# Kernel tuning notes

Measured on AMD Instinct MI355X. Metric: run time of the kernel, lower is better.

Reference implementation:

```python
import jax, jax.numpy as jnp
import numpy as np

N, E, F_IN, F_E, EMB, G = 25000, 100000, 32, 8, 32, 512


def _nnconv(x, src, dst, ea, w1, b1, w2, b2, root, bias):
    # edge MLP: [E,F_E] -> [E,16] -> [E, in*EMB] -> per-edge weight matrix [E,in,EMB]
    h = jax.nn.relu(ea @ w1 + b1)
    W = (h @ w2 + b2).reshape(ea.shape[0], x.shape[1], EMB)
    # gather source nodes, per-edge matmul, scatter-add to targets (PyG NNConv, aggr='add')
    msg = jnp.einsum('ei,eio->eo', x[src], W)
    agg = jax.ops.segment_sum(msg, dst, num_segments=x.shape[0])
    return agg + x @ root + bias


def _branch(x, ei, ea, p0, p1):
    x = jax.nn.relu(_nnconv(x, ei[0], ei[1], ea, *p0))
    x = jax.nn.relu(_nnconv(x, ei[0], ei[1], ea, *p1))
    return x


def setup_inputs() -> dict:
    key = jax.random.key(0)
    ks = iter(jax.random.split(key, 64))
    def rnd(shape, s=1.0):
        return jax.random.normal(next(ks), shape, dtype=jnp.float32) * s
    inp = {
        'x_p': rnd((N, F_IN)), 'x_d': rnd((N, F_IN)),
        'edge_attr_p': rnd((E, F_E)), 'edge_attr_d': rnd((E, F_E)),
        'edge_index_p': jax.random.randint(next(ks), (2, E), 0, N),
        'edge_index_d': jax.random.randint(next(ks), (2, E), 0, N),
        'batch_p': jnp.sort(jax.random.randint(next(ks), (N,), 0, G)),
        'batch_d': jnp.sort(jax.random.randint(next(ks), (N,), 0, G)),
    }
    for b in ('p', 'd'):
        inp[b + '_nn0_w1'] = rnd((F_E, 16), 0.1)
        inp[b + '_nn0_b1'] = rnd((16,), 0.1)
        inp[b + '_nn0_w2'] = rnd((16, F_IN * EMB), 0.1)
        inp[b + '_nn0_b2'] = rnd((F_IN * EMB,), 0.1)
        inp[b + '_root0'] = rnd((F_IN, EMB), 0.1)
        inp[b + '_bias0'] = rnd((EMB,), 0.1)
        inp[b + '_nn1_w1'] = rnd((F_E, 16), 0.1)
        inp[b + '_nn1_b1'] = rnd((16,), 0.1)
        inp[b + '_nn1_w2'] = rnd((16, EMB * EMB), 0.1)
        inp[b + '_nn1_b2'] = rnd((EMB * EMB,), 0.1)
        inp[b + '_root1'] = rnd((EMB, EMB), 0.1)
        inp[b + '_bias1'] = rnd((EMB,), 0.1)
    inp['lin0_w'] = rnd((2 * EMB, 2 * EMB), 0.1)
    inp['lin0_b'] = rnd((2 * EMB,), 0.1)
    inp['lin1_w'] = rnd((2 * EMB, 1), 0.1)
    inp['lin1_b'] = rnd((1,), 0.1)
    return inp


def reference(x_p, x_d, edge_attr_p, edge_attr_d, edge_index_p, edge_index_d, batch_p, batch_d,
              p_nn0_w1, p_nn0_b1, p_nn0_w2, p_nn0_b2, p_root0, p_bias0,
              p_nn1_w1, p_nn1_b1, p_nn1_w2, p_nn1_b2, p_root1, p_bias1,
              d_nn0_w1, d_nn0_b1, d_nn0_w2, d_nn0_b2, d_root0, d_bias0,
              d_nn1_w1, d_nn1_b1, d_nn1_w2, d_nn1_b2, d_root1, d_bias1,
              lin0_w, lin0_b, lin1_w, lin1_b):
    p0 = (p_nn0_w1, p_nn0_b1, p_nn0_w2, p_nn0_b2, p_root0, p_bias0)
    p1 = (p_nn1_w1, p_nn1_b1, p_nn1_w2, p_nn1_b2, p_root1, p_bias1)
    d0 = (d_nn0_w1, d_nn0_b1, d_nn0_w2, d_nn0_b2, d_root0, d_bias0)
    d1 = (d_nn1_w1, d_nn1_b1, d_nn1_w2, d_nn1_b2, d_root1, d_bias1)
    hp = _branch(x_p, edge_index_p, edge_attr_p, p0, p1)      # [N, EMB]
    hd = _branch(x_d, edge_index_d, edge_attr_d, d0, d1)      # [N, EMB]
    gp = jax.ops.segment_max(hp, batch_p, num_segments=G)     # global_max_pool
    gd = jax.ops.segment_max(hd, batch_d, num_segments=G)
    x = jnp.concatenate([gp, gd], axis=1)                     # [G, 2*EMB]
    # F.dropout(p=0.5, training=False) is the identity in eval mode
    x = x @ lin0_w + lin0_b
    x = x @ lin1_w + lin1_b                                    # [G, 1]
    return x
```

## Files before the change

kernel.cpp:

```cpp
#include <hip/hip_runtime.h>
#include <hip/hip_bf16.h>

#define NN 25000
#define NE 100000
#define NG 512
#define NPAD 25024
#define NEP 100032
#define NT 6250
#define XL (2 * NPAD * 32)

typedef __attribute__((ext_vector_type(8))) short short8;
typedef __attribute__((ext_vector_type(4))) float f32x4;

__device__ __forceinline__ float bf2f(unsigned short u) {
    union { unsigned u; float f; } v; v.u = (unsigned)u << 16; return v.f;
}
__device__ __forceinline__ unsigned short f2bf(float f) {
    union { __hip_bfloat16 b; unsigned short u; } c;
    c.b = __float2bfloat16(f);
    return c.u;
}
__device__ __forceinline__ unsigned pk2(float lo, float hi) {
    __hip_bfloat162 h2;
    h2.x = __float2bfloat16(lo);
    h2.y = __float2bfloat16(hi);
    union { __hip_bfloat162 h; unsigned u; } c; c.h = h2; return c.u;
}

struct PrepArgs {
    const float* w2[4]; const float* b2[4];
    const float* x0[2];
};
#define S1 (4 * 17 * 1024)
#define S2V (2 * NN * 8)
#define S3 (2 * NN)
__global__ __launch_bounds__(256) void prep_kernel(PrepArgs pa,
        unsigned short* __restrict__ Wt, unsigned short* __restrict__ xb,
        int* __restrict__ hist) {
    int idx = blockIdx.x * 256 + threadIdx.x;
    if (idx < S1) {
        int L = idx / (17 * 1024);
        int r = idx % (17 * 1024);
        int s = r >> 10, o = (r >> 5) & 31, i = r & 31;
        float v = (s < 16) ? pa.w2[L][s * 1024 + i * 32 + o] : pa.b2[L][i * 32 + o];
        Wt[idx] = f2bf(v);
        return;
    }
    idx -= S1;
    if (idx < S2V) {
        int br = idx / (NN * 8);
        int q = idx % (NN * 8);
        float4 v = *(const float4*)(pa.x0[br] + (size_t)q * 4);
        unsigned* dst = (unsigned*)(xb + (size_t)br * NPAD * 32 + (size_t)q * 4);
        dst[0] = pk2(v.x, v.y);
        dst[1] = pk2(v.z, v.w);
        return;
    }
    idx -= S2V;
    if (idx < S3) hist[idx] = 0;
}

__global__ __launch_bounds__(256) void hist_kernel(const int* __restrict__ ep,
        const int* __restrict__ ed, int* __restrict__ hist, int* __restrict__ slot) {
    int idx = blockIdx.x * 256 + threadIdx.x;
    if (idx >= 2 * NE) return;
    int br = idx >= NE, e = idx - br * NE;
    const int* ei = br ? ed : ep;
    slot[idx] = atomicAdd(&hist[br * NN + ei[NE + e]], 1);
}

__global__ __launch_bounds__(1024) void scan_kernel(const int* __restrict__ hist,
        int* __restrict__ ptr) {
    int br = blockIdx.x, t = threadIdx.x;
    const int* h = hist + br * NN;
    int* p = ptr + br * (NN + 1);
    int base = t * 25;
    int loc[25]; int s = 0;
    if (base < NN) {
        #pragma unroll
        for (int j = 0; j < 25; ++j) { loc[j] = h[base + j]; s += loc[j]; }
    }
    int w = t >> 6, ln = t & 63;
    int v = s;
    #pragma unroll
    for (int d = 1; d < 64; d <<= 1) {
        int u = __shfl_up(v, d, 64);
        if (ln >= d) v += u;
    }
    __shared__ int wsum[16];
    if (ln == 63) wsum[w] = v;
    __syncthreads();
    if (t < 16) {
        int x = wsum[t];
        #pragma unroll
        for (int d = 1; d < 16; d <<= 1) {
            int u = __shfl_up(x, d, 16);
            if ((t & 15) >= d) x += u;
        }
        wsum[t] = x;
    }
    __syncthreads();
    int run = (w ? wsum[w - 1] : 0) + (v - s);
    if (base < NN) {
        #pragma unroll
        for (int j = 0; j < 25; ++j) { p[base + j] = run; run += loc[j]; }
    }
    if (t == 0) p[NN] = wsum[15];
}

struct EdgeArgs {
    const float* ea[2]; const int* eidx[2];
    const float* w1[2]; const float* b1[2];
};
__global__ __launch_bounds__(256, 2) void edge_kernel(EdgeArgs A, int L,
        const unsigned short* __restrict__ Wt,
        const unsigned short* __restrict__ xb,
        const int* __restrict__ ptr, const int* __restrict__ slot,
        unsigned short* __restrict__ msg) {
    __shared__ unsigned tr[4][256];
    int br = blockIdx.x >> 8;
    int bb = blockIdx.x & 255;
    const float* ea   = A.ea[br];
    const int*   eidx = A.eidx[br];
    const float* w1   = A.w1[br];
    const float* b1   = A.b1[br];
    const unsigned short* W  = Wt + (size_t)(br * 2 + L) * 17 * 1024;
    const unsigned short* xc = xb + (size_t)L * XL + (size_t)br * NPAD * 32;
    const int* pt = ptr + br * (NN + 1);
    const int* sl = slot + br * NE;
    unsigned short* mg = msg + (size_t)br * NEP * 32;

    int tid = threadIdx.x;
    int wv = tid >> 6, lane = tid & 63;
    int lr = lane & 15, kg = lane >> 4;

    short8 WA[17], WB[17];
    #pragma unroll
    for (int s = 0; s < 17; ++s) {
        WA[s] = *(const short8*)(W + (size_t)s * 1024 + lr * 32 + kg * 8);
        WB[s] = *(const short8*)(W + (size_t)s * 1024 + (16 + lr) * 32 + kg * 8);
    }
    float w1r[32], b1r[4];
    #pragma unroll
    for (int r = 0; r < 4; ++r) {
        b1r[r] = b1[kg * 4 + r];
        #pragma unroll
        for (int i = 0; i < 8; ++i) w1r[r * 8 + i] = w1[i * 16 + kg * 4 + r];
    }

    for (int t = bb * 4 + wv; t < NT; t += 1024) {
        int e = t * 16 + lr;
        int src = eidx[e];
        int rk = 0;
        if (kg == 0) rk = pt[eidx[NE + e]] + sl[e];

        short8 xs8 = *(const short8*)(xc + (size_t)src * 32 + kg * 8);
        float xf[8];
        #pragma unroll
        for (int j = 0; j < 8; ++j) xf[j] = bf2f((unsigned short)xs8[j]);

        float4 ea0 = *(const float4*)(ea + (size_t)e * 8);
        float4 ea1 = *(const float4*)(ea + (size_t)e * 8 + 4);
        float hreg[4];
        #pragma unroll
        for (int r = 0; r < 4; ++r) {
            float h = b1r[r];
            h += ea0.x * w1r[r * 8 + 0]; h += ea0.y * w1r[r * 8 + 1];
            h += ea0.z * w1r[r * 8 + 2]; h += ea0.w * w1r[r * 8 + 3];
            h += ea1.x * w1r[r * 8 + 4]; h += ea1.y * w1r[r * 8 + 5];
            h += ea1.z * w1r[r * 8 + 6]; h += ea1.w * w1r[r * 8 + 7];
            hreg[r] = fmaxf(h, 0.f);
        }

        f32x4 acc0 = {0.f, 0.f, 0.f, 0.f}, acc1 = {0.f, 0.f, 0.f, 0.f};
        #pragma unroll
        for (int s = 0; s < 17; ++s) {
            short8 y;
            if (s < 16) {
                float hs = __shfl(hreg[s & 3], lr + ((s >> 2) << 4), 64);
                union { unsigned u[4]; short8 v; } yy;
                yy.u[0] = pk2(hs * xf[0], hs * xf[1]);
                yy.u[1] = pk2(hs * xf[2], hs * xf[3]);
                yy.u[2] = pk2(hs * xf[4], hs * xf[5]);
                yy.u[3] = pk2(hs * xf[6], hs * xf[7]);
                y = yy.v;
            } else {
                y = xs8;
            }
            acc0 = __builtin_amdgcn_mfma_f32_16x16x32_bf16(WA[s], y, acc0, 0, 0, 0);
            acc1 = __builtin_amdgcn_mfma_f32_16x16x32_bf16(WB[s], y, acc1, 0, 0, 0);
        }
        tr[wv][lr * 16 + kg * 2    ] = pk2(acc0[0], acc0[1]);
        tr[wv][lr * 16 + kg * 2 + 1] = pk2(acc0[2], acc0[3]);
        tr[wv][lr * 16 + 8 + kg * 2    ] = pk2(acc1[0], acc1[1]);
        tr[wv][lr * 16 + 8 + kg * 2 + 1] = pk2(acc1[2], acc1[3]);
        int rkb = __shfl(rk, lane >> 2, 64);
        uint4 val = *(uint4*)&tr[wv][(lane >> 2) * 16 + (lane & 3) * 4];
        *(uint4*)(mg + (size_t)rkb * 32 + (lane & 3) * 8) = val;
    }
}

struct GatherArgs { const float* root[2]; const float* bias[2]; };
__global__ __launch_bounds__(256) void gather_kernel(GatherArgs G,
        const int* __restrict__ ptr, const unsigned short* __restrict__ msg,
        const unsigned short* __restrict__ xin_, unsigned short* __restrict__ xout_) {
    int gw = (blockIdx.x * 256 + threadIdx.x) >> 5;
    int l = threadIdx.x & 31;
    int br = gw >= NN, n = gw - br * NN;
    const int* p = ptr + br * (NN + 1);
    int lo = p[n], hi = p[n + 1];
    const unsigned short* m = msg + (size_t)br * NEP * 32;
    int sub = l >> 3, q = l & 7;
    float ps0 = 0.f, ps1 = 0.f, ps2 = 0.f, ps3 = 0.f;
    for (int j = lo + sub; j < hi; j += 4) {
        uint2 w = *(const uint2*)(m + (size_t)j * 32 + q * 4);
        ps0 += bf2f((unsigned short)(w.x & 0xffffu));
        ps1 += bf2f((unsigned short)(w.x >> 16));
        ps2 += bf2f((unsigned short)(w.y & 0xffffu));
        ps3 += bf2f((unsigned short)(w.y >> 16));
    }
    ps0 += __shfl_xor(ps0, 8, 64); ps0 += __shfl_xor(ps0, 16, 64);
    ps1 += __shfl_xor(ps1, 8, 64); ps1 += __shfl_xor(ps1, 16, 64);
    ps2 += __shfl_xor(ps2, 8, 64); ps2 += __shfl_xor(ps2, 16, 64);
    ps3 += __shfl_xor(ps3, 8, 64); ps3 += __shfl_xor(ps3, 16, 64);
    int srcl = l >> 2;
    float t0 = __shfl(ps0, srcl, 32);
    float t1 = __shfl(ps1, srcl, 32);
    float t2 = __shfl(ps2, srcl, 32);
    float t3 = __shfl(ps3, srcl, 32);
    int c = l & 3;
    float sum = (c & 2) ? ((c & 1) ? t3 : t2) : ((c & 1) ? t1 : t0);

    float xv = bf2f(xin_[(size_t)br * NPAD * 32 + (size_t)n * 32 + l]);
    const float* R = G.root[br];
    float rsum = 0.f;
    #pragma unroll
    for (int i = 0; i < 32; ++i) rsum += __shfl(xv, i, 32) * R[i * 32 + l];
    float v = fmaxf(sum + rsum + G.bias[br][l], 0.f);
    xout_[(size_t)br * NPAD * 32 + (size_t)n * 32 + l] = f2bf(v);
}

struct SFArgs {
    const int* batch[2];
    const float* lw0; const float* lb0; const float* lw1; const float* lb1;
};
__global__ __launch_bounds__(256) void segmaxfinal_kernel(SFArgs S,
        const unsigned short* __restrict__ x2, float* __restrict__ out) {
    int g = blockIdx.x;
    __shared__ float red[256];
    __shared__ float xg[64];
    int o = threadIdx.x & 31, row = threadIdx.x >> 5;
    for (int brc = 0; brc < 2; ++brc) {
        const int* b = S.batch[brc];
        int lo = 0, hi = NN;
        while (lo < hi) { int mid = (lo + hi) >> 1; if (b[mid] < g) lo = mid + 1; else hi = mid; }
        int s0 = lo;
        hi = NN;
        while (lo < hi) { int mid = (lo + hi) >> 1; if (b[mid] < g + 1) lo = mid + 1; else hi = mid; }
        int s1 = lo;
        const unsigned short* h = x2 + (size_t)brc * NPAD * 32;
        float mv = 0.f;
        for (int n = s0 + row; n < s1; n += 8) mv = fmaxf(mv, bf2f(h[(size_t)n * 32 + o]));
        red[threadIdx.x] = mv; __syncthreads();
        if (row < 4) red[threadIdx.x] = fmaxf(red[threadIdx.x], red[threadIdx.x + 128]);
        __syncthreads();
        if (row < 2) red[threadIdx.x] = fmaxf(red[threadIdx.x], red[threadIdx.x + 64]);
        __syncthreads();
        if (row == 0) xg[brc * 32 + o] = fmaxf(red[threadIdx.x], red[threadIdx.x + 32]);
        __syncthreads();
    }
    if (threadIdx.x < 64) {
        int j = threadIdx.x;
        float y = S.lb0[j];
        for (int i = 0; i < 64; ++i) y += xg[i] * S.lw0[i * 64 + j];
        float t = y * S.lw1[j];
        #pragma unroll
        for (int off = 32; off > 0; off >>= 1) t += __shfl_down(t, off, 64);
        if (j == 0) out[g] = t + S.lb1[0];
    }
}

static size_t aln(size_t v) { return (v + 255) & ~(size_t)255; }

extern "C" void kernel_launch(void* const* d_in, const int* in_sizes, int n_in,
                              void* d_out, int out_size, void* d_ws, size_t ws_size,
                              hipStream_t stream) {
    (void)in_sizes; (void)n_in; (void)out_size; (void)ws_size;
    char* w = (char*)d_ws;
    unsigned short* Wt  = (unsigned short*)w; w += aln((size_t)S1 * 2);
    unsigned short* xb  = (unsigned short*)w; w += aln((size_t)3 * XL * 2);
    unsigned short* msg = (unsigned short*)w; w += aln((size_t)2 * NEP * 32 * 2);
    int* hist = (int*)w; w += aln((size_t)2 * NN * 4);
    int* ptr  = (int*)w; w += aln((size_t)2 * (NN + 1) * 4);
    int* slot = (int*)w; w += aln((size_t)2 * NE * 4);

    const int* ep = (const int*)d_in[4];
    const int* ed = (const int*)d_in[5];

    PrepArgs pa;
    for (int L4 = 0; L4 < 4; ++L4) {
        int base = 8 + (L4 >> 1) * 12 + (L4 & 1) * 6;
        pa.w2[L4] = (const float*)d_in[base + 2];
        pa.b2[L4] = (const float*)d_in[base + 3];
    }
    pa.x0[0] = (const float*)d_in[0];
    pa.x0[1] = (const float*)d_in[1];
    prep_kernel<<<(S1 + S2V + S3 + 255) / 256, 256, 0, stream>>>(pa, Wt, xb, hist);

    hist_kernel<<<(2 * NE + 255) / 256, 256, 0, stream>>>(ep, ed, hist, slot);
    scan_kernel<<<2, 1024, 0, stream>>>(hist, ptr);

    EdgeArgs ea; GatherArgs ga;
    for (int br = 0; br < 2; ++br) {
        ea.ea[br]   = (const float*)d_in[2 + br];
        ea.eidx[br] = (const int*)d_in[4 + br];
    }
    for (int L = 0; L < 2; ++L) {
        for (int br = 0; br < 2; ++br) {
            int base = 8 + br * 12 + L * 6;
            ea.w1[br]   = (const float*)d_in[base + 0];
            ea.b1[br]   = (const float*)d_in[base + 1];
            ga.root[br] = (const float*)d_in[base + 4];
            ga.bias[br] = (const float*)d_in[base + 5];
        }
        edge_kernel<<<512, 256, 0, stream>>>(ea, L, Wt, xb, ptr, slot, msg);
        gather_kernel<<<6250, 256, 0, stream>>>(ga, ptr, msg,
            xb + (size_t)L * XL, xb + (size_t)(L + 1) * XL);
    }

    SFArgs sf;
    sf.batch[0] = (const int*)d_in[6];
    sf.batch[1] = (const int*)d_in[7];
    sf.lw0 = (const float*)d_in[32];
    sf.lb0 = (const float*)d_in[33];
    sf.lw1 = (const float*)d_in[34];
    sf.lb1 = (const float*)d_in[35];
    segmaxfinal_kernel<<<NG, 256, 0, stream>>>(sf, xb + (size_t)2 * XL, (float*)d_out);
}
```

Measured before the change: 119.8 us.

## Store edge messages in edge order and gather via precomputed CSR edge permutation

```diff
diff --git a/kernel.cpp b/kernel.cpp
--- a/kernel.cpp
+++ b/kernel.cpp
@@ -108,6 +108,17 @@
     if (t == 0) p[NN] = wsum[15];
 }
 
+struct ScArgs { const int* eidx[2]; };
+__global__ __launch_bounds__(256) void scatter_kernel(ScArgs A,
+        const int* __restrict__ ptr, const int* __restrict__ slot,
+        int* __restrict__ eord) {
+    int idx = blockIdx.x * 256 + threadIdx.x;
+    if (idx >= 2 * NE) return;
+    int br = idx >= NE, e = idx - br * NE;
+    int dst = A.eidx[br][NE + e];
+    eord[br * NE + ptr[br * (NN + 1) + dst] + slot[idx]] = e;
+}
+
 struct EdgeArgs {
     const float* ea[2]; const int* eidx[2];
     const float* w1[2]; const float* b1[2];
@@ -115,7 +126,6 @@
 __global__ __launch_bounds__(256, 2) void edge_kernel(EdgeArgs A, int L,
         const unsigned short* __restrict__ Wt,
         const unsigned short* __restrict__ xb,
-        const int* __restrict__ ptr, const int* __restrict__ slot,
         unsigned short* __restrict__ msg) {
     __shared__ unsigned tr[4][256];
     int br = blockIdx.x >> 8;
@@ -126,8 +136,6 @@
     const float* b1   = A.b1[br];
     const unsigned short* W  = Wt + (size_t)(br * 2 + L) * 17 * 1024;
     const unsigned short* xc = xb + (size_t)L * XL + (size_t)br * NPAD * 32;
-    const int* pt = ptr + br * (NN + 1);
-    const int* sl = slot + br * NE;
     unsigned short* mg = msg + (size_t)br * NEP * 32;
 
     int tid = threadIdx.x;
@@ -151,8 +159,6 @@
     for (int t = bb * 4 + wv; t < NT; t += 1024) {
         int e = t * 16 + lr;
         int src = eidx[e];
-        int rk = 0;
-        if (kg == 0) rk = pt[eidx[NE + e]] + sl[e];
 
         short8 xs8 = *(const short8*)(xc + (size_t)src * 32 + kg * 8);
         float xf[8];
@@ -194,26 +200,31 @@
         tr[wv][lr * 16 + kg * 2 + 1] = pk2(acc0[2], acc0[3]);
         tr[wv][lr * 16 + 8 + kg * 2    ] = pk2(acc1[0], acc1[1]);
         tr[wv][lr * 16 + 8 + kg * 2 + 1] = pk2(acc1[2], acc1[3]);
-        int rkb = __shfl(rk, lane >> 2, 64);
-        uint4 val = *(uint4*)&tr[wv][(lane >> 2) * 16 + (lane & 3) * 4];
-        *(uint4*)(mg + (size_t)rkb * 32 + (lane & 3) * 8) = val;
+        unsigned* gm = (unsigned*)(mg + (size_t)t * 16 * 32);
+        gm[lane]       = tr[wv][lane];
+        gm[lane + 64]  = tr[wv][lane + 64];
+        gm[lane + 128] = tr[wv][lane + 128];
+        gm[lane + 192] = tr[wv][lane + 192];
     }
 }
 
 struct GatherArgs { const float* root[2]; const float* bias[2]; };
 __global__ __launch_bounds__(256) void gather_kernel(GatherArgs G,
-        const int* __restrict__ ptr, const unsigned short* __restrict__ msg,
+        const int* __restrict__ ptr, const int* __restrict__ eord,
+        const unsigned short* __restrict__ msg,
         const unsigned short* __restrict__ xin_, unsigned short* __restrict__ xout_) {
     int gw = (blockIdx.x * 256 + threadIdx.x) >> 5;
     int l = threadIdx.x & 31;
     int br = gw >= NN, n = gw - br * NN;
     const int* p = ptr + br * (NN + 1);
     int lo = p[n], hi = p[n + 1];
+    const int* eo = eord + br * NE;
     const unsigned short* m = msg + (size_t)br * NEP * 32;
     int sub = l >> 3, q = l & 7;
     float ps0 = 0.f, ps1 = 0.f, ps2 = 0.f, ps3 = 0.f;
     for (int j = lo + sub; j < hi; j += 4) {
-        uint2 w = *(const uint2*)(m + (size_t)j * 32 + q * 4);
+        int e = eo[j];
+        uint2 w = *(const uint2*)(m + (size_t)e * 32 + q * 4);
         ps0 += bf2f((unsigned short)(w.x & 0xffffu));
         ps1 += bf2f((unsigned short)(w.x >> 16));
         ps2 += bf2f((unsigned short)(w.y & 0xffffu));
@@ -293,6 +304,7 @@
     int* hist = (int*)w; w += aln((size_t)2 * NN * 4);
     int* ptr  = (int*)w; w += aln((size_t)2 * (NN + 1) * 4);
     int* slot = (int*)w; w += aln((size_t)2 * NE * 4);
+    int* eord = (int*)w; w += aln((size_t)2 * NE * 4);
 
     const int* ep = (const int*)d_in[4];
     const int* ed = (const int*)d_in[5];
@@ -309,6 +321,11 @@
 
     hist_kernel<<<(2 * NE + 255) / 256, 256, 0, stream>>>(ep, ed, hist, slot);
     scan_kernel<<<2, 1024, 0, stream>>>(hist, ptr);
+
+    ScArgs sc;
+    sc.eidx[0] = ep;
+    sc.eidx[1] = ed;
+    scatter_kernel<<<(2 * NE + 255) / 256, 256, 0, stream>>>(sc, ptr, slot, eord);
 
     EdgeArgs ea; GatherArgs ga;
     for (int br = 0; br < 2; ++br) {
@@ -323,8 +340,8 @@
             ga.root[br] = (const float*)d_in[base + 4];
             ga.bias[br] = (const float*)d_in[base + 5];
         }
-        edge_kernel<<<512, 256, 0, stream>>>(ea, L, Wt, xb, ptr, slot, msg);
-        gather_kernel<<<6250, 256, 0, stream>>>(ga, ptr, msg,
+        edge_kernel<<<512, 256, 0, stream>>>(ea, L, Wt, xb, msg);
+        gather_kernel<<<6250, 256, 0, stream>>>(ga, ptr, eord, msg,
             xb + (size_t)L * XL, xb + (size_t)(L + 1) * XL);
     }
 
```

New measurement: 131.4 us. +9.7%, slower.
